# Performance work log

Measured on AMD Instinct MI355X. Metric: run time of the kernel, lower is better.

Reference implementation:

```python
import jax, jax.numpy as jnp
import numpy as np

B, C, H, W = 32, 64, 64, 64
K, D = 512, 64  # num_embeddings, embedding_dim (C == D)


def setup_inputs() -> dict:
    key = jax.random.key(0)
    k1, k2 = jax.random.split(key)
    z_e = jax.random.normal(k1, (B, C, H, W), dtype=jnp.float32)
    # torch init: uniform_(-1/K, 1/K)
    codebook = jax.random.uniform(k2, (K, D), dtype=jnp.float32,
                                  minval=-1.0 / K, maxval=1.0 / K)
    return {"z_e": z_e, "codebook": codebook}


def reference(z_e, codebook):
    # [B,C,H,W] -> [B,H,W,C] -> [N,C]
    z_flat = jnp.transpose(z_e, (0, 2, 3, 1)).reshape(-1, z_e.shape[1])
    distances = (jnp.sum(z_flat ** 2, axis=1, keepdims=True)
                 + jnp.sum(codebook ** 2, axis=1)
                 - 2.0 * jnp.matmul(z_flat, codebook.T))
    encoding_indices = jnp.argmin(distances, axis=1)  # [N]
    z_q_flat = codebook[encoding_indices]             # [N,D]
    # NOTE: original torch code does z_q_flat.view(z_e.shape) WITHOUT
    # inverse permute; replicate that raw reinterpretation exactly.
    z_q = z_q_flat.reshape(z_e.shape)
    return z_q, encoding_indices
```

## Files before the change

### kernel.cpp

```cpp
#include <hip/hip_runtime.h>


typedef __attribute__((ext_vector_type(4))) float fl4;

__global__ __launch_bounds__(256)
void vq13a(const float* __restrict__ z, float* __restrict__ ow)
{
    __shared__ float zl[256][65];
    const int tid = threadIdx.x;
    const int n0  = blockIdx.x << 8;
    const int n   = n0 + tid;
    const size_t base = (size_t)(n >> 12) * 262144 + (size_t)(n & 4095);

    float p[8];
    #pragma unroll
    for (int c = 0; c < 64; ++c) {
        const float v = z[base + (size_t)c * 4096];
        zl[tid][c] = v;
        const float sq = __fmul_rn(v, v);
        if (c < 8) p[c] = sq;
        else       p[c & 7] = __fadd_rn(p[c & 7], sq);
    }
    const float s1 = __fadd_rn(__fadd_rn(__fadd_rn(p[0],p[1]),__fadd_rn(p[2],p[3])),
                               __fadd_rn(__fadd_rn(p[4],p[5]),__fadd_rn(p[6],p[7])));
    ow[8388608 + n] = s1;
    __syncthreads();

    float* zt = ow + (size_t)n0 * 64;
    #pragma unroll
    for (int j = 0; j < 16; ++j) {
        const int f  = j * 256 + tid;
        const int nl = f >> 4, c0 = (f & 15) << 2;
        fl4 v;
        #pragma unroll
        for (int e = 0; e < 4; ++e) v[e] = zl[nl][c0 + e];
        *(fl4*)(zt + ((size_t)f << 2)) = v;
    }
}

#define CBE(i) cbv[(i) >> 2][(i) & 3]

__global__ __launch_bounds__(512, 4)
void vq13b(const float* __restrict__ cb,
           const float* __restrict__ zt,
           const float* __restrict__ s1g,
           float* __restrict__ ow)
{
    __shared__ float s1l[128];
    __shared__ float cdl[8][128];
    __shared__ int   ckl[8][128];
    __shared__ int   ifin[128];

    const int tid  = threadIdx.x;
    const int w    = tid >> 6;
    const int lane = tid & 63;
    const int n0   = blockIdx.x << 7;
    const int k    = (w << 6) + lane;

    fl4 cbv[16];
    {
        const fl4* rp = (const fl4*)(cb + ((size_t)k << 6));
        #pragma unroll
        for (int j = 0; j < 16; ++j) cbv[j] = rp[j];
    }
    float s2k;
    {
        float q[8];
        #pragma unroll
        for (int j = 0; j < 8; ++j) q[j] = __fmul_rn(CBE(j), CBE(j));
        #pragma unroll
        for (int m = 1; m < 8; ++m)
            #pragma unroll
            for (int j = 0; j < 8; ++j) {
                const float v = CBE(m * 8 + j);
                q[j] = __fadd_rn(q[j], __fmul_rn(v, v));
            }
        s2k = __fadd_rn(__fadd_rn(__fadd_rn(q[0],q[1]),__fadd_rn(q[2],q[3])),
                        __fadd_rn(__fadd_rn(q[4],q[5]),__fadd_rn(q[6],q[7])));
    }

    if (tid < 128) s1l[tid] = s1g[n0 + tid];
    __syncthreads();

    for (int s = 0; s < 128; ++s) {
        const float* zr = zt + ((size_t)(n0 + s) << 6);
        float m = 0.0f;
        #pragma unroll
        for (int c = 0; c < 64; ++c)
            m = fmaf(zr[c], CBE(c), m);
        const float T = __fadd_rn(s1l[s], s2k);
        const float d = __fsub_rn(T, 2.0f * m);

        float dm = d;
        #pragma unroll
        for (int off = 1; off < 64; off <<= 1)
            dm = fminf(dm, __shfl_xor(dm, off, 64));
        const unsigned long long eq = __ballot(d == dm);
        if (lane == 0) {
            cdl[w][s] = dm;
            ckl[w][s] = (w << 6) + (__ffsll((long long)eq) - 1);
        }
    }
    __syncthreads();

    if (tid < 128) {
        float bd = cdl[0][tid]; int bk = ckl[0][tid];
        #pragma unroll
        for (int ww = 1; ww < 8; ++ww) {
            const float dw = cdl[ww][tid];
            const int   kw = ckl[ww][tid];
            if (dw < bd) { bd = dw; bk = kw; }
        }
        ifin[tid] = bk;
        ow[8388608 + n0 + tid] = (float)bk;
    }
    __syncthreads();

    float* ob = ow + ((size_t)n0 << 6);
    #pragma unroll
    for (int it = 0; it < 4; ++it) {
        const int o    = it * 2048 + (tid << 2);
        const int sloc = o >> 6;
        const int c0   = o & 63;
        const int idx  = ifin[sloc] & 511;
        const fl4 v = *(const fl4*)(cb + ((size_t)idx << 6) + c0);
        *(fl4*)(ob + o) = v;
    }
}

extern "C" void kernel_launch(void* const* d_in, const int* in_sizes, int n_in,
                              void* d_out, int out_size, void* d_ws, size_t ws_size,
                              hipStream_t stream) {
    const float* z  = (const float*)d_in[0];
    const float* cb = (const float*)d_in[1];
    float* out = (float*)d_out;
    vq13a<<<512, 256, 0, stream>>>(z, out);
    vq13b<<<1024, 512, 0, stream>>>(cb, out, out + 8388608, out);
}
```

Before: 264.4 us.

## Hand-write distance loop in inline asm with z in VGPRs and codebook via scalar loads

The distance kernel now has each thread own one z row, held in 64 VGPRs, while the codebook is streamed through SGPRs with s_load_dwordx16 so every FMA uses a scalar operand. The block covers 256 rows, and the two halves of the block each scan 256 codes, replacing the per-sample wave shuffle reduction and ballot with a running per-thread argmin. This removes the repeated global/L1 reads of the z row and the cross-lane reductions in the inner loop. In exchange it relies on hand-written assembly with hard-coded registers, manual waitcnt handling and a fixed trip count. Any clash between those hard-coded registers and the compiler's allocation would give wrong results.

```diff
diff --git a/kernel.cpp b/kernel.cpp
--- a/kernel.cpp
+++ b/kernel.cpp
@@ -4,7 +4,7 @@
 typedef __attribute__((ext_vector_type(4))) float fl4;
 
 __global__ __launch_bounds__(256)
-void vq13a(const float* __restrict__ z, float* __restrict__ ow)
+void vq23a(const float* __restrict__ z, float* __restrict__ ow)
 {
     __shared__ float zl[256][65];
     const int tid = threadIdx.x;
@@ -38,79 +38,186 @@
     }
 }
 
-#define CBE(i) cbv[(i) >> 2][(i) & 3]
+#define F2(SA,SB,VZ) \
+    "v_fmac_f32 v32, s" #SA ", v" #VZ "\n\t" \
+    "v_fmac_f32 v33, s" #SB ", v" #VZ "\n\t"
+#define CH_B0_V40 \
+    F2(36,52,40) F2(37,53,41) F2(38,54,42) F2(39,55,43) \
+    F2(40,56,44) F2(41,57,45) F2(42,58,46) F2(43,59,47) \
+    F2(44,60,48) F2(45,61,49) F2(46,62,50) F2(47,63,51) \
+    F2(48,64,52) F2(49,65,53) F2(50,66,54) F2(51,67,55)
+#define CH_B1_V56 \
+    F2(68,84,56) F2(69,85,57) F2(70,86,58) F2(71,87,59) \
+    F2(72,88,60) F2(73,89,61) F2(74,90,62) F2(75,91,63) \
+    F2(76,92,64) F2(77,93,65) F2(78,94,66) F2(79,95,67) \
+    F2(80,96,68) F2(81,97,69) F2(82,98,70) F2(83,99,71)
+#define CH_B0_V72 \
+    F2(36,52,72) F2(37,53,73) F2(38,54,74) F2(39,55,75) \
+    F2(40,56,76) F2(41,57,77) F2(42,58,78) F2(43,59,79) \
+    F2(44,60,80) F2(45,61,81) F2(46,62,82) F2(47,63,83) \
+    F2(48,64,84) F2(49,65,85) F2(50,66,86) F2(51,67,87)
+#define CH_B1_V88 \
+    F2(68,84,88)  F2(69,85,89)  F2(70,86,90)  F2(71,87,91) \
+    F2(72,88,92)  F2(73,89,93)  F2(74,90,94)  F2(75,91,95) \
+    F2(76,92,96)  F2(77,93,97)  F2(78,94,98)  F2(79,95,99) \
+    F2(80,96,100) F2(81,97,101) F2(82,98,102) F2(83,99,103)
+#define LD_C0 \
+    "s_load_dwordx16 s[36:51], s[34:35], 0x0\n\t" \
+    "s_load_dwordx16 s[52:67], s[34:35], 0x100\n\t"
+#define LD_C1 \
+    "s_load_dwordx16 s[68:83], s[34:35], 0x40\n\t" \
+    "s_load_dwordx16 s[84:99], s[34:35], 0x140\n\t"
+#define LD_C2 \
+    "s_load_dwordx16 s[36:51], s[34:35], 0x80\n\t" \
+    "s_load_dwordx16 s[52:67], s[34:35], 0x180\n\t"
+#define LD_C3 \
+    "s_load_dwordx16 s[68:83], s[34:35], 0xC0\n\t" \
+    "s_load_dwordx16 s[84:99], s[34:35], 0x1C0\n\t"
+#define TAIL \
+    "v_add_f32 v26, %[s1v], v22\n\t" \
+    "v_add_f32 v27, %[s1v], v23\n\t" \
+    "v_fma_f32 v26, v32, -2.0, v26\n\t" \
+    "v_fma_f32 v27, v33, -2.0, v27\n\t" \
+    "v_cmp_lt_f32 vcc, v26, v24\n\t" \
+    "v_cndmask_b32 v24, v24, v26, vcc\n\t" \
+    "v_cndmask_b32 v25, v25, v28, vcc\n\t" \
+    "v_add_u32 v28, 1, v28\n\t" \
+    "v_cmp_lt_f32 vcc, v27, v24\n\t" \
+    "v_cndmask_b32 v24, v24, v27, vcc\n\t" \
+    "v_cndmask_b32 v25, v25, v28, vcc\n\t" \
+    "v_add_u32 v28, 1, v28\n\t" \
+    "v_add_u32 v30, 8, v30\n\t"
+#define PAIR_HEAD \
+    "s_waitcnt lgkmcnt(0)\n\t" \
+    "v_mov_b32 v32, 0\n\t" \
+    "v_mov_b32 v33, 0\n\t" \
+    "ds_read_b64 v[22:23], v30\n\t" \
+    LD_C1 \
+    CH_B0_V40 \
+    "s_waitcnt lgkmcnt(0)\n\t" \
+    LD_C2 \
+    CH_B1_V56 \
+    "s_waitcnt lgkmcnt(0)\n\t" \
+    LD_C3 \
+    CH_B0_V72 \
+    "s_waitcnt lgkmcnt(0)\n\t"
 
 __global__ __launch_bounds__(512, 4)
-void vq13b(const float* __restrict__ cb,
+void vq23b(const float* __restrict__ cb,
            const float* __restrict__ zt,
            const float* __restrict__ s1g,
            float* __restrict__ ow)
 {
-    __shared__ float s1l[128];
-    __shared__ float cdl[8][128];
-    __shared__ int   ckl[8][128];
-    __shared__ int   ifin[128];
+    __shared__ __align__(16) float s2l[512];
+    __shared__ __align__(16) float md[2][256];
+    __shared__ __align__(16) int   mk[2][256];
+    __shared__ int   ifin[256];
 
     const int tid  = threadIdx.x;
     const int w    = tid >> 6;
     const int lane = tid & 63;
-    const int n0   = blockIdx.x << 7;
-    const int k    = (w << 6) + lane;
-
-    fl4 cbv[16];
+    const int g    = w & 3;
+    const int h    = w >> 2;
+    const int n0   = blockIdx.x << 8;
+    const int sloc = (g << 6) + lane;
+    const int n    = n0 + sloc;
+
     {
-        const fl4* rp = (const fl4*)(cb + ((size_t)k << 6));
-        #pragma unroll
-        for (int j = 0; j < 16; ++j) cbv[j] = rp[j];
-    }
-    float s2k;
-    {
+        const float* row = cb + ((size_t)tid << 6);
         float q[8];
         #pragma unroll
-        for (int j = 0; j < 8; ++j) q[j] = __fmul_rn(CBE(j), CBE(j));
+        for (int j = 0; j < 8; ++j) q[j] = __fmul_rn(row[j], row[j]);
         #pragma unroll
         for (int m = 1; m < 8; ++m)
             #pragma unroll
-            for (int j = 0; j < 8; ++j) {
-                const float v = CBE(m * 8 + j);
-                q[j] = __fadd_rn(q[j], __fmul_rn(v, v));
-            }
-        s2k = __fadd_rn(__fadd_rn(__fadd_rn(q[0],q[1]),__fadd_rn(q[2],q[3])),
-                        __fadd_rn(__fadd_rn(q[4],q[5]),__fadd_rn(q[6],q[7])));
-    }
-
-    if (tid < 128) s1l[tid] = s1g[n0 + tid];
-    __syncthreads();
-
-    for (int s = 0; s < 128; ++s) {
-        const float* zr = zt + ((size_t)(n0 + s) << 6);
-        float m = 0.0f;
-        #pragma unroll
-        for (int c = 0; c < 64; ++c)
-            m = fmaf(zr[c], CBE(c), m);
-        const float T = __fadd_rn(s1l[s], s2k);
-        const float d = __fsub_rn(T, 2.0f * m);
-
-        float dm = d;
-        #pragma unroll
-        for (int off = 1; off < 64; off <<= 1)
-            dm = fminf(dm, __shfl_xor(dm, off, 64));
-        const unsigned long long eq = __ballot(d == dm);
-        if (lane == 0) {
-            cdl[w][s] = dm;
-            ckl[w][s] = (w << 6) + (__ffsll((long long)eq) - 1);
-        }
-    }
-    __syncthreads();
-
-    if (tid < 128) {
-        float bd = cdl[0][tid]; int bk = ckl[0][tid];
-        #pragma unroll
-        for (int ww = 1; ww < 8; ++ww) {
-            const float dw = cdl[ww][tid];
-            const int   kw = ckl[ww][tid];
-            if (dw < bd) { bd = dw; bk = kw; }
-        }
+            for (int j = 0; j < 8; ++j)
+                q[j] = __fadd_rn(q[j], __fmul_rn(row[m*8+j], row[m*8+j]));
+        s2l[tid] = __fadd_rn(__fadd_rn(__fadd_rn(q[0],q[1]),__fadd_rn(q[2],q[3])),
+                             __fadd_rn(__fadd_rn(q[4],q[5]),__fadd_rn(q[6],q[7])));
+    }
+
+    const float  s1v = s1g[n];
+    const float* zp  = zt + ((size_t)n << 6);
+    const int    hof = h << 16;
+    unsigned s2a = (unsigned)(unsigned long long)&s2l[h << 8];
+    unsigned mda = (unsigned)(unsigned long long)&md[h][sloc];
+    unsigned mka = (unsigned)(unsigned long long)&mk[h][sloc];
+    const int k0i = h << 8;
+
+    __syncthreads();
+
+    asm volatile(
+        "v_readfirstlane_b32 s30, %[hof]\n\t"
+        "s_add_u32 s34, %[cbp0], s30\n\t"
+        "s_addc_u32 s35, %[cbp1], 0\n\t"
+        "s_movk_i32 s33, 127\n\t"
+        "v_mov_b32 v28, %[k0i]\n\t"
+        "v_mov_b32 v30, %[s2a]\n\t"
+        "v_mov_b32 v24, 0x7f7fffff\n\t"
+        "v_mov_b32 v25, 0\n\t"
+        "global_load_dwordx4 v[40:43],  %[za], off\n\t"
+        "global_load_dwordx4 v[44:47],  %[za], off offset:16\n\t"
+        "global_load_dwordx4 v[48:51],  %[za], off offset:32\n\t"
+        "global_load_dwordx4 v[52:55],  %[za], off offset:48\n\t"
+        "global_load_dwordx4 v[56:59],  %[za], off offset:64\n\t"
+        "global_load_dwordx4 v[60:63],  %[za], off offset:80\n\t"
+        "global_load_dwordx4 v[64:67],  %[za], off offset:96\n\t"
+        "global_load_dwordx4 v[68:71],  %[za], off offset:112\n\t"
+        "global_load_dwordx4 v[72:75],  %[za], off offset:128\n\t"
+        "global_load_dwordx4 v[76:79],  %[za], off offset:144\n\t"
+        "global_load_dwordx4 v[80:83],  %[za], off offset:160\n\t"
+        "global_load_dwordx4 v[84:87],  %[za], off offset:176\n\t"
+        "global_load_dwordx4 v[88:91],  %[za], off offset:192\n\t"
+        "global_load_dwordx4 v[92:95],  %[za], off offset:208\n\t"
+        "global_load_dwordx4 v[96:99],  %[za], off offset:224\n\t"
+        "global_load_dwordx4 v[100:103],%[za], off offset:240\n\t"
+        LD_C0
+        "s_waitcnt vmcnt(0)\n\t"
+        "1:\n\t"
+        PAIR_HEAD
+        "s_add_u32 s34, s34, 0x200\n\t"
+        "s_addc_u32 s35, s35, 0\n\t"
+        LD_C0
+        CH_B1_V88
+        TAIL
+        "s_sub_i32 s33, s33, 1\n\t"
+        "s_cmp_lg_u32 s33, 0\n\t"
+        "s_cbranch_scc1 1b\n\t"
+        PAIR_HEAD
+        CH_B1_V88
+        TAIL
+        "ds_write_b32 %[mda], v24\n\t"
+        "ds_write_b32 %[mka], v25\n\t"
+        :
+        : [cbp0] "s"((unsigned)(unsigned long long)cb),
+          [cbp1] "s"((unsigned)((unsigned long long)cb >> 32)),
+          [hof] "v"(hof), [k0i] "v"(k0i), [za] "v"(zp), [s1v] "v"(s1v),
+          [s2a] "v"(s2a), [mda] "v"(mda), [mka] "v"(mka)
+        : "memory", "vcc", "s30","s33","s34","s35",
+          "s36","s37","s38","s39","s40","s41","s42","s43","s44","s45",
+          "s46","s47","s48","s49","s50","s51","s52","s53","s54","s55",
+          "s56","s57","s58","s59","s60","s61","s62","s63","s64","s65",
+          "s66","s67","s68","s69","s70","s71","s72","s73","s74","s75",
+          "s76","s77","s78","s79","s80","s81","s82","s83","s84","s85",
+          "s86","s87","s88","s89","s90","s91","s92","s93","s94","s95",
+          "s96","s97","s98","s99",
+          "v22","v23","v24","v25","v26","v27","v28","v30","v32","v33",
+          "v40","v41","v42","v43","v44","v45","v46","v47",
+          "v48","v49","v50","v51","v52","v53","v54","v55",
+          "v56","v57","v58","v59","v60","v61","v62","v63",
+          "v64","v65","v66","v67","v68","v69","v70","v71",
+          "v72","v73","v74","v75","v76","v77","v78","v79",
+          "v80","v81","v82","v83","v84","v85","v86","v87",
+          "v88","v89","v90","v91","v92","v93","v94","v95",
+          "v96","v97","v98","v99","v100","v101","v102","v103");
+
+    __syncthreads();
+
+    if (tid < 256) {
+        float bd = md[0][tid]; int bk = mk[0][tid];
+        const float d1 = md[1][tid];
+        const int   k1 = mk[1][tid];
+        if (d1 < bd) { bd = d1; bk = k1; }
         ifin[tid] = bk;
         ow[8388608 + n0 + tid] = (float)bk;
     }
@@ -118,11 +225,11 @@
 
     float* ob = ow + ((size_t)n0 << 6);
     #pragma unroll
-    for (int it = 0; it < 4; ++it) {
+    for (int it = 0; it < 8; ++it) {
         const int o    = it * 2048 + (tid << 2);
-        const int sloc = o >> 6;
+        const int sl   = o >> 6;
         const int c0   = o & 63;
-        const int idx  = ifin[sloc] & 511;
+        const int idx  = ifin[sl] & 511;
         const fl4 v = *(const fl4*)(cb + ((size_t)idx << 6) + c0);
         *(fl4*)(ob + o) = v;
     }
@@ -134,6 +241,6 @@
     const float* z  = (const float*)d_in[0];
     const float* cb = (const float*)d_in[1];
     float* out = (float*)d_out;
-    vq13a<<<512, 256, 0, stream>>>(z, out);
-    vq13b<<<1024, 512, 0, stream>>>(cb, out, out + 8388608, out);
+    vq23a<<<512, 256, 0, stream>>>(z, out);
+    vq23b<<<512, 512, 0, stream>>>(cb, out, out + 8388608, out);
 }
```

New measurement: 225.8 us. 1.17x faster.
